# Optimization experiments

Hardware: AMD Instinct MI355X
Metric: run time of the kernel (lower is better)

The kernel has to match this reference:

```python
import jax, jax.numpy as jnp
import numpy as np

NUM_LEVELS = 4
RADIUS = 4
H, W = 64, 128


def _bilinear_sample(feat, x, y):
    # feat: [N, Hl, Wl]; x, y: [N, K, K] pixel coords; zeros padding, align_corners=True
    N, Hl, Wl = feat.shape
    x0 = jnp.floor(x)
    y0 = jnp.floor(y)
    x1 = x0 + 1.0
    y1 = y0 + 1.0
    wx1 = x - x0
    wx0 = 1.0 - wx1
    wy1 = y - y0
    wy0 = 1.0 - wy1
    n_idx = jnp.arange(N)[:, None, None]

    def gather(xi, yi):
        inb = (xi >= 0) & (xi <= Wl - 1) & (yi >= 0) & (yi <= Hl - 1)
        xc = jnp.clip(xi, 0, Wl - 1).astype(jnp.int32)
        yc = jnp.clip(yi, 0, Hl - 1).astype(jnp.int32)
        v = feat[n_idx, yc, xc]
        return jnp.where(inb, v, jnp.zeros((), feat.dtype))

    return (gather(x0, y0) * wx0 * wy0 + gather(x1, y0) * wx1 * wy0
            + gather(x0, y1) * wx0 * wy1 + gather(x1, y1) * wx1 * wy1)


def _correlation(fmap1, fmap2, coords):
    bs, dim, h, w = fmap1.shape
    f1 = fmap1.reshape(bs, dim, h * w)
    f2 = fmap2.reshape(bs, dim, h * w)
    cv = jnp.einsum('bdm,bdn->bmn', f1, f2) / jnp.sqrt(jnp.asarray(dim, jnp.float32))
    cv = cv.reshape(bs * h * w, h, w)
    pyramid = [cv]
    for _ in range(NUM_LEVELS - 1):
        N, hl, wl = cv.shape
        cv = cv.reshape(N, hl // 2, 2, wl // 2, 2).mean(axis=(2, 4))  # avg_pool2d(2,2)
        pyramid.append(cv)

    cxy = coords.transpose(0, 2, 3, 1).astype(jnp.float32)  # [bs,h,w,2]
    cx = cxy[..., 0].reshape(-1)  # [bs*h*w]
    cy = cxy[..., 1].reshape(-1)
    r = RADIUS
    d = jnp.linspace(-r, r, 2 * r + 1, dtype=jnp.float32)
    dy, dx = jnp.meshgrid(d, d, indexing='ij')  # [K,K]

    outs = []
    for i, corr in enumerate(pyramid):
        scale = jnp.float32(2 ** i)
        x = cx[:, None, None] / scale + dx[None]
        y = cy[:, None, None] / scale + dy[None]
        sampled = _bilinear_sample(corr, x, y)  # [bs*h*w, K, K]
        outs.append(sampled.reshape(bs, h, w, -1))
    out = jnp.concatenate(outs, axis=-1)  # [bs,h,w,num_levels*K*K]
    return out.transpose(0, 3, 1, 2)


def setup_inputs() -> dict:
    key = jax.random.key(0)
    k1, k2, k3, k4 = jax.random.split(key, 4)
    fmap1 = jax.random.normal(k1, (1, 256, H, W), dtype=jnp.float32)
    fmap2 = jax.random.normal(k2, (1, 256, H, W), dtype=jnp.float32)
    cx = jax.random.uniform(k3, (1, 1, H, W), dtype=jnp.float32) * (W - 1)
    cy = jax.random.uniform(k4, (1, 1, H, W), dtype=jnp.float32) * (H - 1)
    coords = jnp.concatenate([cx, cy], axis=1)  # [1,2,H,W], channel 0 = x, 1 = y
    return {"fmap1": fmap1, "fmap2": fmap2, "coords": coords}


def reference(fmap1, fmap2, coords):
    return _correlation(fmap1, fmap2, coords)
```

## Files before the change

### kernel.cpp

```cpp
#include <hip/hip_runtime.h>
#include <stdint.h>

typedef _Float16 f16;
typedef __attribute__((ext_vector_type(8))) _Float16 f16x8;
typedef __attribute__((ext_vector_type(4))) float f32x4;
typedef __attribute__((ext_vector_type(2))) float fv2;
typedef __attribute__((ext_vector_type(4))) float fv4;

#define H0 64
#define W0 128
#define NPIX 8192
#define KD 256
#define NCAT 10880
#define OFF1 8192
#define OFF2 10240
#define OFF3 10752
#define CAP0 640
#define CAP1 2048
#define PL1OFF (32 * CAP0)
#define PLTOT (PL1OFF + 8 * CAP1)
#define ZTOT (64 + PLTOT + 64)


__global__ __launch_bounds__(256) void fused_pre(const float* __restrict__ in0,
                                                 const float* __restrict__ in1,
                                                 f16* __restrict__ At,
                                                 f16* __restrict__ Bt,
                                                 int* __restrict__ cnt) {
  __shared__ f16 tile[64][65];
  int bid = blockIdx.x;
  int t = threadIdx.x;

  if (bid < 1024) {
    const float* in = (bid < 512) ? in0 : in1;
    f16* out = (bid < 512) ? At : Bt;
    size_t NR = (bid < 512) ? NPIX : NCAT;
    int bx = bid & 511;
    int m0 = (bx & 127) * 64;
    int d0 = (bx >> 7) * 64;
    int a = t & 63, b = t >> 6;
#pragma unroll
    for (int i = 0; i < 16; ++i) {
      int d = b + i * 4;
      tile[a][d] = (f16)in[(size_t)(d0 + d) * NPIX + m0 + a];
    }
    __syncthreads();
#pragma unroll
    for (int i = 0; i < 16; ++i) {
      int m = b + i * 4;
      int d = d0 + a;
      out[((size_t)(d >> 5) * NR + (m0 + m)) * 32 + (d & 31)] = tile[m][a];
    }
  } else if (bid < 1360) {
    int idx = (bid - 1024) * 256 + t;
    float acc[8] = {0, 0, 0, 0, 0, 0, 0, 0};
    int r, dc;
    if (idx < 65536) {
      int r1 = idx & 2047; dc = idx >> 11; r = r1;
      int y = r1 >> 6, x = r1 & 63;
#pragma unroll
      for (int e = 0; e < 8; ++e) {
        const float* p = in1 + (size_t)(dc * 8 + e) * NPIX + (y * 2) * W0 + x * 2;
        fv2 s0 = *(const fv2*)p;
        fv2 s1 = *(const fv2*)(p + W0);
        acc[e] = (s0[0] + s0[1] + s1[0] + s1[1]) * 0.25f;
      }
    } else if (idx < 81920) {
      int i2 = idx - 65536;
      int r2 = i2 & 511; dc = i2 >> 9; r = 2048 + r2;
      int y = r2 >> 5, x = r2 & 31;
#pragma unroll
      for (int e = 0; e < 8; ++e) {
        const float* p = in1 + (size_t)(dc * 8 + e) * NPIX + (y * 4) * W0 + x * 4;
        float s = 0.f;
#pragma unroll
        for (int h = 0; h < 4; ++h) {
          fv4 v = *(const fv4*)(p + h * W0);
          s += v[0] + v[1] + v[2] + v[3];
        }
        acc[e] = s * 0.0625f;
      }
    } else {
      int i3 = idx - 81920;
      int r3 = i3 & 127; dc = i3 >> 7; r = 2560 + r3;
      int y = r3 >> 4, x = r3 & 15;
#pragma unroll
      for (int e = 0; e < 8; ++e) {
        const float* p = in1 + (size_t)(dc * 8 + e) * NPIX + (y * 8) * W0 + x * 8;
        float s = 0.f;
#pragma unroll
        for (int h = 0; h < 8; ++h) {
          fv4 v0 = *(const fv4*)(p + h * W0);
          fv4 v1 = *(const fv4*)(p + h * W0 + 4);
          s += v0[0] + v0[1] + v0[2] + v0[3] + v1[0] + v1[1] + v1[2] + v1[3];
        }
        acc[e] = s * 0.015625f;
      }
    }
    f16x8 o;
#pragma unroll
    for (int e = 0; e < 8; ++e) o[e] = (f16)acc[e];
    *(f16x8*)(Bt + ((size_t)(dc >> 2) * NCAT + 8192 + r) * 32 + (dc & 3) * 8) = o;
  } else {
    int idx = (bid - 1360) * 256 + t;
    if (idx < ZTOT) cnt[idx] = 0;
  }
}

__global__ __launch_bounds__(1024) void bucket_build(const float* __restrict__ coords,
                                                     int2* __restrict__ meta,
                                                     int* __restrict__ cnt) {
  __shared__ int hist[40];
  __shared__ int base[40];
  int* plist = cnt + 64;
  int t = threadIdx.x;
  int m = blockIdx.x * 1024 + t;
  if (t < 40) hist[t] = 0;
  __syncthreads();

  float cx = coords[m];
  float cy = coords[NPIX + m];
  int X0l[2], Y0l[2];
  int mx = 0, my = 0;
#pragma unroll
  for (int lev = 0; lev < 4; ++lev) {
    float inv = 1.0f / (float)(1 << lev);
    int X0 = (int)floorf(cx * inv) - 4;
    int Y0 = (int)floorf(cy * inv) - 4;
    if (lev < 2) { X0l[lev] = X0; Y0l[lev] = Y0; }
    mx |= (X0 & 0xff) << (8 * lev);
    my |= (Y0 & 0xff) << (8 * lev);
  }
  meta[m] = make_int2(mx, my);

  int b0 = (min(max(Y0l[0], 0), 63) >> 4) * 8 + (min(max(X0l[0], 0), 127) >> 4);
  int b1 = (min(max(Y0l[1], 0), 31) >> 4) * 4 + (min(max(X0l[1], 0), 63) >> 4);
  int s0 = atomicAdd(&hist[b0], 1);
  int s1 = atomicAdd(&hist[32 + b1], 1);
  __syncthreads();

  if (t < 40) base[t] = atomicAdd(&cnt[t], hist[t]);
  __syncthreads();

  int p0 = base[b0] + s0;
  if (p0 < CAP0) plist[b0 * CAP0 + p0] = m;
  int p1 = base[32 + b1] + s1;
  if (p1 < CAP1) plist[PL1OFF + b1 * CAP1 + p1] = m;
}

__global__ __launch_bounds__(256, 2) void gemm_all(const f16* __restrict__ At,
                                                   const f16* __restrict__ Bt,
                                                   const int* __restrict__ cnt,
                                                   const int2* __restrict__ meta,
                                                   f16* __restrict__ Wbuf) {
  const int* plist = cnt + 64;
  int bid = blockIdx.x;
  int t = threadIdx.x;
  int lane = t & 63;
  int w = t >> 6;
  int lr = lane & 15;
  int ko = lane >> 4;

  if (bid < 160) {
    int bm = (((bid & 7) << 2) | ((bid >> 3) & 3)) << 8;
    int bn = OFF2 + ((bid >> 5) << 7);

    const f16* Ab = At + (size_t)(bm + w * 64 + lr) * 32 + ko * 8;
    const f16* Bb = Bt + (size_t)(bn + lr) * 32 + ko * 8;

    f16x8 af[2][4], bf[2][8];
#define LOADK(s, kk)                                                           \
    do {                                                                       \
      const f16* ap = Ab + (size_t)(kk) * (NPIX * 32);                         \
      const f16* bp = Bb + (size_t)(kk) * (NCAT * 32);                         \
      _Pragma("unroll")                                                        \
      for (int i = 0; i < 4; ++i) af[s][i] = *(const f16x8*)(ap + i * 512);    \
      _Pragma("unroll")                                                        \
      for (int i = 0; i < 8; ++i) bf[s][i] = *(const f16x8*)(bp + i * 512);    \
    } while (0)

    f32x4 acc[4][8];
#pragma unroll
    for (int i = 0; i < 4; ++i)
#pragma unroll
      for (int j = 0; j < 8; ++j) acc[i][j] = (f32x4){0.f, 0.f, 0.f, 0.f};

    LOADK(0, 0);
    LOADK(1, 1);
#pragma unroll
    for (int kk = 0; kk < 8; ++kk) {
      const int cur = kk & 1;
#pragma unroll
      for (int mi = 0; mi < 4; ++mi)
#pragma unroll
        for (int ni = 0; ni < 8; ++ni)
          acc[mi][ni] = __builtin_amdgcn_mfma_f32_16x16x32_f16(
              af[cur][mi], bf[cur][ni], acc[mi][ni], 0, 0, 0);
      if (kk + 2 < 8) LOADK(cur, kk + 2);
    }
#undef LOADK

    int lev, n0, wlog;
    if (bn < OFF3) { lev = 2; n0 = bn - OFF2; wlog = 5; }
    else           { lev = 3; n0 = bn - OFF3; wlog = 4; }
    int wmask = (1 << wlog) - 1;
    int yA = n0 >> wlog;
    int yB = (n0 + 127) >> wlog;
    int ycol[8], xcol[8];
#pragma unroll
    for (int ni = 0; ni < 8; ++ni) {
      int n = n0 + ni * 16 + lr;
      ycol[ni] = n >> wlog;
      xcol[ni] = n & wmask;
    }
    f16* wlev = Wbuf + (size_t)(lev * 100) * NPIX;
    int sh = lev * 8;
#pragma unroll
    for (int mi = 0; mi < 4; ++mi)
#pragma unroll
      for (int r2 = 0; r2 < 4; ++r2) {
        int grow = bm + w * 64 + mi * 16 + ko * 4 + r2;
        int2 mv = meta[grow];
        int Y0 = (int)(signed char)((mv.y >> sh) & 0xff);
        if (Y0 <= yB && Y0 + 9 >= yA) {
          int X0 = (int)(signed char)((mv.x >> sh) & 0xff);
          f16* rowp = wlev + grow;
#pragma unroll
          for (int ni = 0; ni < 8; ++ni) {
            int dy = ycol[ni] - Y0;
            int dx = xcol[ni] - X0;
            if ((unsigned)dy < 10u && (unsigned)dx < 10u)
              rowp[(size_t)(dy * 10 + dx) * NPIX] =
                  (f16)(acc[mi][ni][r2] * 0.0625f);
          }
        }
      }
    return;
  }

  int bb = bid - 160;
  int lev, b, mg, half;
  if (bb < 1280) { lev = 0; b = bb / 40; int r = bb % 40; mg = r >> 1; half = r & 1; }
  else { lev = 1; int i = bb - 1280; b = i / 128; int r = i % 128; mg = r >> 1; half = r & 1; }

  int CAP   = lev ? CAP1 : CAP0;
  int cb    = min(cnt[lev ? 32 + b : b], CAP);
  if (mg * 32 >= cb) return;
  int Hl    = lev ? 32 : 64;
  int Wmap  = lev ? 64 : 128;
  int bx    = lev ? (b & 3) : (b & 7);
  int by    = lev ? (b >> 2) : (b >> 3);
  int x0 = bx * 16, y0 = by * 16;
  int NY = min(25, Hl - y0);
  int rowbase = lev ? 8192 : 0;
  int pbase = (lev ? PL1OFF + b * CAP1 : b * CAP0) + mg * 32;

  int prow[2];
  prow[0] = plist[pbase + lr] & (NPIX - 1);
  prow[1] = plist[pbase + 16 + lr] & (NPIX - 1);

  bool vst[4];
  int brow[4];
#pragma unroll
  for (int st = 0; st < 4; ++st) {
    int q = w + 4 * st;
    int yl = half * 13 + q;
    vst[st] = (q < (half ? 12 : 13)) && (yl < NY);
    int ylc = min(yl, NY - 1);
    brow[st] = rowbase + (y0 + ylc) * Wmap + x0 + lr;
  }

  f16x8 af[2][2], bf[2][8];
#define BLD(s_, kk_)                                                           \
  do {                                                                         \
    const f16* ap = At + (size_t)(kk_) * (NPIX * 32) + ko * 8;                 \
    const f16* bp = Bt + (size_t)(kk_) * (NCAT * 32) + ko * 8;                 \
    af[s_][0] = *(const f16x8*)(ap + prow[0] * 32);                            \
    af[s_][1] = *(const f16x8*)(ap + prow[1] * 32);                            \
    _Pragma("unroll")                                                          \
    for (int st = 0; st < 4; ++st) {                                           \
      bf[s_][st * 2]     = *(const f16x8*)(bp + (size_t)brow[st] * 32);        \
      bf[s_][st * 2 + 1] = *(const f16x8*)(bp + (size_t)(brow[st] + 16) * 32); \
    }                                                                          \
  } while (0)

  f32x4 acc[8][2];
#pragma unroll
  for (int i = 0; i < 8; ++i)
#pragma unroll
    for (int j = 0; j < 2; ++j) acc[i][j] = (f32x4){0.f, 0.f, 0.f, 0.f};

  BLD(0, 0);
  BLD(1, 1);
#pragma unroll
  for (int kk = 0; kk < 8; ++kk) {
    const int cur = kk & 1;
#pragma unroll
    for (int nf = 0; nf < 8; ++nf)
#pragma unroll
      for (int mi = 0; mi < 2; ++mi)
        acc[nf][mi] = __builtin_amdgcn_mfma_f32_16x16x32_f16(
            af[cur][mi], bf[cur][nf], acc[nf][mi], 0, 0, 0);
    if (kk + 2 < 8) BLD(cur, kk + 2);
  }
#undef BLD

  int pe[2][4];
  int Xp[2][4], Yp[2][4];
  int sh = lev * 8;
#pragma unroll
  for (int mi = 0; mi < 2; ++mi)
#pragma unroll
    for (int r2 = 0; r2 < 4; ++r2) {
      int slot = mg * 32 + mi * 16 + ko * 4 + r2;
      int p = plist[pbase + mi * 16 + ko * 4 + r2] & (NPIX - 1);
      pe[mi][r2] = (slot < cb) ? p : -1;
      int2 mv = meta[p];
      Xp[mi][r2] = (int)(signed char)((mv.x >> sh) & 0xff);
      Yp[mi][r2] = (int)(signed char)((mv.y >> sh) & 0xff);
    }
  f16* wl = Wbuf + (size_t)(lev * 100) * NPIX;
#pragma unroll
  for (int st = 0; st < 4; ++st) {
    if (!vst[st]) continue;
    int y = y0 + half * 13 + w + 4 * st;
#pragma unroll
    for (int xc = 0; xc < 2; ++xc) {
      int x = x0 + xc * 16 + lr;
#pragma unroll
      for (int mi = 0; mi < 2; ++mi)
#pragma unroll
        for (int r2 = 0; r2 < 4; ++r2) {
          int p = pe[mi][r2];
          int dy = y - Yp[mi][r2];
          int dx = x - Xp[mi][r2];
          if (p >= 0 && (unsigned)dy < 10u && (unsigned)dx < 10u)
            wl[(size_t)(dy * 10 + dx) * NPIX + p] =
                (f16)(acc[st * 2 + xc][mi][r2] * 0.0625f);
        }
    }
  }
}

__global__ __launch_bounds__(256) void corr_sample(const f16* __restrict__ Wbuf,
                                                   const float* __restrict__ coords,
                                                   float* __restrict__ out) {
  int bx = blockIdx.x;
  int xcd = bx & 7;
  int idx = bx >> 3;
  int j = idx % 9;
  int mc = xcd + 8 * (idx / 9);
  int m = mc * 256 + threadIdx.x;
  int lev = blockIdx.z;
  int Hl = H0 >> lev, Wl = W0 >> lev;

  float cx = coords[m];
  float cy = coords[NPIX + m];
  float inv = 1.0f / (float)(1 << lev);
  float xb = cx * inv, yb = cy * inv;
  float fx = floorf(xb), fy = floorf(yb);
  int X0 = (int)fx - 4, Y0 = (int)fy - 4;
  float wx1 = xb - fx, wx0 = 1.0f - wx1;
  float wy1 = yb - fy, wy0 = 1.0f - wy1;

  const f16* wb = Wbuf + (size_t)(lev * 100) * NPIX + m;
  float* op = out + ((size_t)lev * 81 + (size_t)j * 9) * NPIX + m;

  float cur[10], nxt[10];
  auto loadrow = [&](float* row, int jr) {
    int y = Y0 + jr;
    bool yin = (unsigned)y < (unsigned)Hl;
#pragma unroll
    for (int i = 0; i < 10; ++i) {
      int x = X0 + i;
      bool in = yin && ((unsigned)x < (unsigned)Wl);
      row[i] = in ? (float)wb[(size_t)(jr * 10 + i) * NPIX] : 0.0f;
    }
  };
  loadrow(cur, j);
  loadrow(nxt, j + 1);
#pragma unroll
  for (int i = 0; i < 9; ++i) {
    float v = wy0 * (wx0 * cur[i] + wx1 * cur[i + 1])
            + wy1 * (wx0 * nxt[i] + wx1 * nxt[i + 1]);
    op[(size_t)i * NPIX] = v;
  }
}

extern "C" void kernel_launch(void* const* d_in, const int* in_sizes, int n_in,
                              void* d_out, int out_size, void* d_ws, size_t ws_size,
                              hipStream_t stream) {
  const float* fmap1  = (const float*)d_in[0];
  const float* fmap2  = (const float*)d_in[1];
  const float* coords = (const float*)d_in[2];
  float* out = (float*)d_out;

  char* ws = (char*)d_ws;
  size_t offA = 0;
  size_t offB = offA + (size_t)NPIX * KD * 2;
  size_t offW = offB + (size_t)NCAT * KD * 2;
  size_t offM = offW + (size_t)400 * NPIX * 2;
  size_t offC = offM + (size_t)NPIX * 8;
  size_t need = offC + (size_t)ZTOT * 4;
  if (ws_size < need) return;

  f16*  At   = (f16*)(ws + offA);
  f16*  Bt   = (f16*)(ws + offB);
  f16*  Wbuf = (f16*)(ws + offW);
  int2* meta = (int2*)(ws + offM);
  int*  cnt  = (int*)(ws + offC);

  fused_pre<<<1505, 256, 0, stream>>>(fmap1, fmap2, At, Bt, cnt);
  bucket_build<<<8, 1024, 0, stream>>>(coords, meta, cnt);
  gemm_all<<<2464, 256, 0, stream>>>(At, Bt, cnt, meta, Wbuf);
  corr_sample<<<dim3(288, 1, 4), 256, 0, stream>>>(Wbuf, coords, out);
}
```

Baseline: 82.43 us.

## Store window buffer per-pixel contiguous and stage gathered A rows in LDS

The intermediate correlation window buffer moves from a level/offset-major layout (stride NPIX per window cell) to a per-pixel layout of 512 halves, with 128 per level and 12-wide rows. The sampler then reads a pixel's whole window with vector loads and computes all 81 outputs per thread, replacing strided scalar gathers. In the bucketed GEMM path, the gathered A rows for the 32 pixels are staged once into XOR-swizzled shared memory instead of being reloaded from global per k-step. The costs are scattered 2-byte writes in the GEMM epilogue, a much smaller sampler grid with heavy per-thread register use, and an extra barrier.

Result: faster. 73.35 us (-11.0%).

```diff
diff --git a/kernel.cpp b/kernel.cpp
--- a/kernel.cpp
+++ b/kernel.cpp
@@ -153,6 +153,7 @@
                                                    const int* __restrict__ cnt,
                                                    const int2* __restrict__ meta,
                                                    f16* __restrict__ Wbuf) {
+  __shared__ f16 sa[8192];
   const int* plist = cnt + 64;
   int bid = blockIdx.x;
   int t = threadIdx.x;
@@ -213,7 +214,6 @@
       ycol[ni] = n >> wlog;
       xcol[ni] = n & wmask;
     }
-    f16* wlev = Wbuf + (size_t)(lev * 100) * NPIX;
     int sh = lev * 8;
 #pragma unroll
     for (int mi = 0; mi < 4; ++mi)
@@ -224,14 +224,13 @@
         int Y0 = (int)(signed char)((mv.y >> sh) & 0xff);
         if (Y0 <= yB && Y0 + 9 >= yA) {
           int X0 = (int)(signed char)((mv.x >> sh) & 0xff);
-          f16* rowp = wlev + grow;
+          f16* rowp = Wbuf + (size_t)grow * 512 + lev * 128;
 #pragma unroll
           for (int ni = 0; ni < 8; ++ni) {
             int dy = ycol[ni] - Y0;
             int dx = xcol[ni] - X0;
             if ((unsigned)dy < 10u && (unsigned)dx < 10u)
-              rowp[(size_t)(dy * 10 + dx) * NPIX] =
-                  (f16)(acc[mi][ni][r2] * 0.0625f);
+              rowp[dy * 12 + dx] = (f16)(acc[mi][ni][r2] * 0.0625f);
           }
         }
       }
@@ -255,9 +254,29 @@
   int rowbase = lev ? 8192 : 0;
   int pbase = (lev ? PL1OFF + b * CAP1 : b * CAP0) + mg * 32;
 
-  int prow[2];
-  prow[0] = plist[pbase + lr] & (NPIX - 1);
-  prow[1] = plist[pbase + 16 + lr] & (NPIX - 1);
+  {
+    int spix = t >> 3;
+    int skk  = t & 7;
+    int sp = plist[pbase + spix] & (NPIX - 1);
+    const f16* g = At + (size_t)skk * (NPIX * 32) + (size_t)sp * 32;
+    int line = spix >> 1;
+    int sb = (spix & 1) * 4;
+    f16* dst = sa + skk * 1024 + line * 64;
+#pragma unroll
+    for (int q = 0; q < 4; ++q) {
+      int phys = (sb + q) ^ (line & 7);
+      *(f16x8*)(dst + phys * 8) = *(const f16x8*)(g + q * 8);
+    }
+  }
+
+  int aoff[2];
+#pragma unroll
+  for (int mi = 0; mi < 2; ++mi) {
+    int pl = mi * 16 + lr;
+    int line = pl >> 1;
+    int phys = ((pl & 1) * 4 + ko) ^ (line & 7);
+    aoff[mi] = line * 64 + phys * 8;
+  }
 
   bool vst[4];
   int brow[4];
@@ -270,13 +289,10 @@
     brow[st] = rowbase + (y0 + ylc) * Wmap + x0 + lr;
   }
 
-  f16x8 af[2][2], bf[2][8];
-#define BLD(s_, kk_)                                                           \
+  f16x8 bf[2][8];
+#define BLDB(s_, kk_)                                                          \
   do {                                                                         \
-    const f16* ap = At + (size_t)(kk_) * (NPIX * 32) + ko * 8;                 \
     const f16* bp = Bt + (size_t)(kk_) * (NCAT * 32) + ko * 8;                 \
-    af[s_][0] = *(const f16x8*)(ap + prow[0] * 32);                            \
-    af[s_][1] = *(const f16x8*)(ap + prow[1] * 32);                            \
     _Pragma("unroll")                                                          \
     for (int st = 0; st < 4; ++st) {                                           \
       bf[s_][st * 2]     = *(const f16x8*)(bp + (size_t)brow[st] * 32);        \
@@ -284,26 +300,32 @@
     }                                                                          \
   } while (0)
 
+  BLDB(0, 0);
+  BLDB(1, 1);
+
   f32x4 acc[8][2];
 #pragma unroll
   for (int i = 0; i < 8; ++i)
 #pragma unroll
     for (int j = 0; j < 2; ++j) acc[i][j] = (f32x4){0.f, 0.f, 0.f, 0.f};
 
-  BLD(0, 0);
-  BLD(1, 1);
+  __syncthreads();
+
 #pragma unroll
   for (int kk = 0; kk < 8; ++kk) {
     const int cur = kk & 1;
-#pragma unroll
-    for (int nf = 0; nf < 8; ++nf)
-#pragma unroll
-      for (int mi = 0; mi < 2; ++mi)
-        acc[nf][mi] = __builtin_amdgcn_mfma_f32_16x16x32_f16(
-            af[cur][mi], bf[cur][nf], acc[nf][mi], 0, 0, 0);
-    if (kk + 2 < 8) BLD(cur, kk + 2);
-  }
-#undef BLD
+    f16x8 a0 = *(const f16x8*)(sa + kk * 1024 + aoff[0]);
+    f16x8 a1 = *(const f16x8*)(sa + kk * 1024 + aoff[1]);
+#pragma unroll
+    for (int nf = 0; nf < 8; ++nf) {
+      acc[nf][0] = __builtin_amdgcn_mfma_f32_16x16x32_f16(a0, bf[cur][nf],
+                                                          acc[nf][0], 0, 0, 0);
+      acc[nf][1] = __builtin_amdgcn_mfma_f32_16x16x32_f16(a1, bf[cur][nf],
+                                                          acc[nf][1], 0, 0, 0);
+    }
+    if (kk + 2 < 8) BLDB(cur, kk + 2);
+  }
+#undef BLDB
 
   int pe[2][4];
   int Xp[2][4], Yp[2][4];
@@ -319,7 +341,6 @@
       Xp[mi][r2] = (int)(signed char)((mv.x >> sh) & 0xff);
       Yp[mi][r2] = (int)(signed char)((mv.y >> sh) & 0xff);
     }
-  f16* wl = Wbuf + (size_t)(lev * 100) * NPIX;
 #pragma unroll
   for (int st = 0; st < 4; ++st) {
     if (!vst[st]) continue;
@@ -335,23 +356,19 @@
           int dy = y - Yp[mi][r2];
           int dx = x - Xp[mi][r2];
           if (p >= 0 && (unsigned)dy < 10u && (unsigned)dx < 10u)
-            wl[(size_t)(dy * 10 + dx) * NPIX + p] =
+            Wbuf[(size_t)p * 512 + lev * 128 + dy * 12 + dx] =
                 (f16)(acc[st * 2 + xc][mi][r2] * 0.0625f);
         }
     }
   }
 }
 
-__global__ __launch_bounds__(256) void corr_sample(const f16* __restrict__ Wbuf,
-                                                   const float* __restrict__ coords,
-                                                   float* __restrict__ out) {
-  int bx = blockIdx.x;
-  int xcd = bx & 7;
-  int idx = bx >> 3;
-  int j = idx % 9;
-  int mc = xcd + 8 * (idx / 9);
-  int m = mc * 256 + threadIdx.x;
-  int lev = blockIdx.z;
+__global__ __launch_bounds__(64) void corr_sample(const f16* __restrict__ Wbuf,
+                                                  const float* __restrict__ coords,
+                                                  float* __restrict__ out) {
+  int tid = blockIdx.x * 64 + threadIdx.x;
+  int m = tid & (NPIX - 1);
+  int lev = tid >> 13;
   int Hl = H0 >> lev, Wl = W0 >> lev;
 
   float cx = coords[m];
@@ -363,27 +380,35 @@
   float wx1 = xb - fx, wx0 = 1.0f - wx1;
   float wy1 = yb - fy, wy0 = 1.0f - wy1;
 
-  const f16* wb = Wbuf + (size_t)(lev * 100) * NPIX + m;
-  float* op = out + ((size_t)lev * 81 + (size_t)j * 9) * NPIX + m;
-
-  float cur[10], nxt[10];
-  auto loadrow = [&](float* row, int jr) {
-    int y = Y0 + jr;
-    bool yin = (unsigned)y < (unsigned)Hl;
-#pragma unroll
-    for (int i = 0; i < 10; ++i) {
-      int x = X0 + i;
-      bool in = yin && ((unsigned)x < (unsigned)Wl);
-      row[i] = in ? (float)wb[(size_t)(jr * 10 + i) * NPIX] : 0.0f;
-    }
-  };
-  loadrow(cur, j);
-  loadrow(nxt, j + 1);
-#pragma unroll
-  for (int i = 0; i < 9; ++i) {
-    float v = wy0 * (wx0 * cur[i] + wx1 * cur[i + 1])
-            + wy1 * (wx0 * nxt[i] + wx1 * nxt[i + 1]);
-    op[(size_t)i * NPIX] = v;
+  const f16* wb = Wbuf + (size_t)m * 512 + lev * 128;
+  f16x8 rv[15];
+#pragma unroll
+  for (int i = 0; i < 15; ++i) rv[i] = *(const f16x8*)(wb + i * 8);
+
+  float* op = out + (size_t)lev * 81 * NPIX + m;
+  float cur[11], nxt[11];
+#pragma unroll
+  for (int i = 0; i < 11; ++i) {
+    bool in = ((unsigned)Y0 < (unsigned)Hl) && ((unsigned)(X0 + i) < (unsigned)Wl);
+    cur[i] = in ? (float)rv[i >> 3][i & 7] : 0.0f;
+  }
+#pragma unroll
+  for (int j = 0; j < 9; ++j) {
+    bool yin = (unsigned)(Y0 + j + 1) < (unsigned)Hl;
+#pragma unroll
+    for (int i = 0; i < 11; ++i) {
+      int c = (j + 1) * 12 + i;
+      bool in = yin && ((unsigned)(X0 + i) < (unsigned)Wl);
+      nxt[i] = in ? (float)rv[c >> 3][c & 7] : 0.0f;
+    }
+#pragma unroll
+    for (int i = 0; i < 9; ++i) {
+      float v = wy0 * (wx0 * cur[i] + wx1 * cur[i + 1])
+              + wy1 * (wx0 * nxt[i] + wx1 * nxt[i + 1]);
+      op[(size_t)(j * 9 + i) * NPIX] = v;
+    }
+#pragma unroll
+    for (int i = 0; i < 11; ++i) cur[i] = nxt[i];
   }
 }
 
@@ -399,7 +424,7 @@
   size_t offA = 0;
   size_t offB = offA + (size_t)NPIX * KD * 2;
   size_t offW = offB + (size_t)NCAT * KD * 2;
-  size_t offM = offW + (size_t)400 * NPIX * 2;
+  size_t offM = offW + (size_t)NPIX * 512 * 2;
   size_t offC = offM + (size_t)NPIX * 8;
   size_t need = offC + (size_t)ZTOT * 4;
   if (ws_size < need) return;
@@ -413,5 +438,5 @@
   fused_pre<<<1505, 256, 0, stream>>>(fmap1, fmap2, At, Bt, cnt);
   bucket_build<<<8, 1024, 0, stream>>>(coords, meta, cnt);
   gemm_all<<<2464, 256, 0, stream>>>(At, Bt, cnt, meta, Wbuf);
-  corr_sample<<<dim3(288, 1, 4), 256, 0, stream>>>(Wbuf, coords, out);
+  corr_sample<<<512, 64, 0, stream>>>(Wbuf, coords, out);
 }
```
